# Performance work log

Hardware: AMD Instinct MI355X
Metric: run time of the kernel (lower is better)

## Reference

```python
import jax, jax.numpy as jnp
import numpy as np

B, C, H, W = 16, 512, 64, 64
L, D = 77, 768
NH = 8
HD = C // NH
EPS = 1e-5


def layernorm(x, g, b):
    m = jnp.mean(x, axis=-1, keepdims=True)
    v = jnp.var(x, axis=-1, keepdims=True)
    return (x - m) * jax.lax.rsqrt(v + EPS) * g + b


def setup_inputs() -> dict:
    key = jax.random.key(0)
    ks = jax.random.split(key, 12)
    s_c = 1.0 / np.sqrt(C)
    s_d = 1.0 / np.sqrt(D)
    return {
        "x": jax.random.normal(ks[0], (B, C, H, W), jnp.float32),
        "text_features": jax.random.normal(ks[1], (B, L, D), jnp.float32),
        "wq": jax.random.normal(ks[2], (C, C), jnp.float32) * s_c,
        "bq": jnp.zeros((C,), jnp.float32),
        "wk": jax.random.normal(ks[3], (C, D), jnp.float32) * s_d,
        "bk": jnp.zeros((C,), jnp.float32),
        "wv": jax.random.normal(ks[4], (C, D), jnp.float32) * s_d,
        "bv": jnp.zeros((C,), jnp.float32),
        "wo": jax.random.normal(ks[5], (C, C), jnp.float32) * s_c,
        "bo": jnp.zeros((C,), jnp.float32),
        "g1": jnp.ones((C,), jnp.float32),
        "b1": jnp.zeros((C,), jnp.float32),
        "g2": jnp.ones((C,), jnp.float32),
        "b2": jnp.zeros((C,), jnp.float32),
    }


def reference(x, text_features, wq, bq, wk, bk, wv, bv, wo, bo, g1, b1, g2, b2):
    b, c, h, w = x.shape
    # 1x1 conv query projection
    q = jnp.einsum('bchw,oc->bohw', x, wq) + bq[None, :, None, None]
    # 2D positional encoding: first c/2 channels vary along w, next c/2 along h
    pos_x = jnp.broadcast_to(jnp.linspace(0.0, 1.0, w)[None, :], (h, w))
    pos_y = jnp.broadcast_to(jnp.linspace(0.0, 1.0, h)[:, None], (h, w))
    pe = jnp.concatenate([
        jnp.broadcast_to(pos_x[None], (c // 2, h, w)),
        jnp.broadcast_to(pos_y[None], (c // 2, h, w)),
    ], axis=0)  # [C,H,W]
    q = q + 0.05 * pe[None]
    # flatten spatial -> tokens, layernorm over channels
    q_flat = q.reshape(b, c, h * w).transpose(0, 2, 1)  # [B,HW,C]
    q_norm = layernorm(q_flat, g1, b1)
    qh = q_norm.reshape(b, h * w, NH, HD)  # [B,HW,NH,HD]
    # text key/value projections
    k = jnp.einsum('bld,cd->blc', text_features, wk) + bk
    v = jnp.einsum('bld,cd->blc', text_features, wv) + bv
    k_norm = layernorm(k, g2, b2)
    kh = k_norm.reshape(b, -1, NH, HD)
    vh = v.reshape(b, -1, NH, HD)
    scale = HD ** -0.5
    attn = jnp.einsum('bqhd,bkhd->bhqk', qh, kh) * scale  # [B,NH,HW,L]
    attn = jax.nn.softmax(attn, axis=-1)  # dropout is identity in eval
    out = jnp.einsum('bhqk,bkhd->bqhd', attn, vh).reshape(b, h * w, c)
    out = out.transpose(0, 2, 1).reshape(b, c, h, w)
    out = jnp.einsum('bchw,oc->bohw', out, wo) + bo[None, :, None, None]
    return out + x
```

## Files before the change

kernel.cpp:

```cpp
#include <hip/hip_runtime.h>
#include <stdint.h>

#define BD   16
#define CD   512
#define HD_  64
#define NH_  8
#define HWD  4096
#define LD   77
#define DD   768

typedef __bf16 bf16;
typedef bf16 bf16x8 __attribute__((ext_vector_type(8)));
typedef float f32x4 __attribute__((ext_vector_type(4)));

__device__ __forceinline__ void async16(const bf16* g, bf16* l) {
  __builtin_amdgcn_global_load_lds(
      (const __attribute__((address_space(1))) void*)g,
      (__attribute__((address_space(3))) void*)l, 16, 0, 0);
}

__device__ __forceinline__ unsigned short bfb(float f) {
  bf16 h = (bf16)f;
  return __builtin_bit_cast(unsigned short, h);
}

__global__ __launch_bounds__(256) void xpose_cvt(const float* __restrict__ X,
                                                 bf16* __restrict__ Y) {
  __shared__ float tile[64][68];
  const int b = blockIdx.z, c0 = blockIdx.y * 64, t0 = blockIdx.x * 64;
  const int tid = threadIdx.x;
  const float* Xb = X + ((size_t)b * CD + c0) * HWD + t0;
#pragma unroll
  for (int p = 0; p < 4; ++p) {
    int c = (tid >> 4) + p * 16;
    int t = (tid & 15) * 4;
    float4 v = *(const float4*)(Xb + (size_t)c * HWD + t);
    *(float4*)&tile[c][t] = v;
  }
  __syncthreads();
  int t = tid >> 2, cb = (tid & 3) * 16;
  union { uint4 u[2]; unsigned short us[16]; } pk;
#pragma unroll
  for (int j = 0; j < 16; ++j) pk.us[j] = bfb(tile[cb + j][t]);
  uint4* Yp = (uint4*)(Y + ((size_t)(b * HWD + t0 + t)) * CD + c0 + cb);
  Yp[0] = pk.u[0];
  Yp[1] = pk.u[1];
}

__global__ __launch_bounds__(256) void cvt_all(
    const float* __restrict__ t, const float* __restrict__ q,
    const float* __restrict__ k, const float* __restrict__ v,
    const float* __restrict__ o, bf16* __restrict__ tb, bf16* __restrict__ qb,
    bf16* __restrict__ kb, bf16* __restrict__ vb, bf16* __restrict__ ob) {
  int bid = blockIdx.x;
  const float* src;
  bf16* dst;
  if (bid < 462) { src = t; dst = tb; }
  else if (bid < 590) { src = q; dst = qb; bid -= 462; }
  else if (bid < 782) { src = k; dst = kb; bid -= 590; }
  else if (bid < 974) { src = v; dst = vb; bid -= 782; }
  else { src = o; dst = ob; bid -= 974; }
  int i = (bid * 256 + threadIdx.x) * 8;
  float4 a = *(const float4*)(src + i);
  float4 c = *(const float4*)(src + i + 4);
  union { uint4 u; unsigned short us[8]; } pk;
  pk.us[0] = bfb(a.x); pk.us[1] = bfb(a.y); pk.us[2] = bfb(a.z); pk.us[3] = bfb(a.w);
  pk.us[4] = bfb(c.x); pk.us[5] = bfb(c.y); pk.us[6] = bfb(c.z); pk.us[7] = bfb(c.w);
  *(uint4*)(dst + i) = pk.u;
}

template <int TM, int TN, int MODE>
__global__ __launch_bounds__(256)
void gemm_bt(const bf16* __restrict__ A, const bf16* __restrict__ B,
             int M, int N, int K,
             const float* __restrict__ bias, const float* __restrict__ xres,
             float* __restrict__ D,
             const bf16* __restrict__ B2, const float* __restrict__ bias2,
             float* __restrict__ D2) {
  constexpr int WM = TM / 2, WN = TN / 2;
  constexpr int AFR = WM / 16, BFR = WN / 16;
  constexpr int ACH = TM / 8, TCH = (TM + TN) / 8, WCH = TCH / 4;
  __shared__ bf16 sA[TM * 64];
  __shared__ bf16 sB[TN * 64];
  const int tid = threadIdx.x, wave = tid >> 6, lane = tid & 63;
  const int m0 = blockIdx.y * TM;
  int n0 = blockIdx.x * TN;
  if constexpr (MODE == 2) {
    if (n0 >= (N >> 1)) { B = B2; bias = bias2; D = D2; n0 -= (N >> 1); }
  }
  const int wm = (wave >> 1) * WM, wn = (wave & 1) * WN;
  const int sub = lane >> 3, col8 = (lane & 7) * 8;
  const int mlo = lane & 15, khi = lane >> 4;
  f32x4 acc[AFR][BFR] = {};

  for (int k0 = 0; k0 < K; k0 += 64) {
#pragma unroll
    for (int r = 0; r < WCH; ++r) {
      int ci = wave * WCH + r;
      if (ci < ACH) {
        int row = ci * 8 + sub;
        int g = m0 + row;
        if (g > M - 1) g = M - 1;
        async16(A + (size_t)g * K + k0 + col8, &sA[ci * 512]);
      } else {
        int cj = ci - ACH;
        int row = cj * 8 + sub;
        async16(B + (size_t)(n0 + row) * K + k0 + col8, &sB[cj * 512]);
      }
    }
    __syncthreads();
#pragma unroll
    for (int kc = 0; kc < 2; ++kc) {
      bf16x8 af[AFR], bfv[BFR];
      const int ko = kc * 32 + khi * 8;
#pragma unroll
      for (int i = 0; i < AFR; ++i)
        af[i] = *(const bf16x8*)&sA[(wm + i * 16 + mlo) * 64 + ko];
#pragma unroll
      for (int j = 0; j < BFR; ++j)
        bfv[j] = *(const bf16x8*)&sB[(wn + j * 16 + mlo) * 64 + ko];
#pragma unroll
      for (int i = 0; i < AFR; ++i)
#pragma unroll
        for (int j = 0; j < BFR; ++j)
          acc[i][j] = __builtin_amdgcn_mfma_f32_16x16x32_bf16(af[i], bfv[j],
                                                              acc[i][j], 0, 0, 0);
    }
    __syncthreads();
  }

  if constexpr (MODE == 3) {
    float bn[BFR];
#pragma unroll
    for (int j = 0; j < BFR; ++j) bn[j] = bias[n0 + wn + j * 16 + mlo];
#pragma unroll
    for (int i = 0; i < AFR; ++i) {
      const int m = m0 + wm + i * 16 + khi * 4;
      const int b = m >> 12, hw = m & (HWD - 1);
      const float* xr0 = xres + ((size_t)b * CD) * HWD + hw;
      float* d0 = D + ((size_t)b * CD) * HWD + hw;
#pragma unroll
      for (int j = 0; j < BFR; ++j) {
        const size_t off = (size_t)(n0 + wn + j * 16 + mlo) * HWD;
        float4 xr = *(const float4*)(xr0 + off);
        float4 ov;
        ov.x = acc[i][j][0] + bn[j] + xr.x;
        ov.y = acc[i][j][1] + bn[j] + xr.y;
        ov.z = acc[i][j][2] + bn[j] + xr.z;
        ov.w = acc[i][j][3] + bn[j] + xr.w;
        *(float4*)(d0 + off) = ov;
      }
    }
  } else {
#pragma unroll
    for (int i = 0; i < AFR; ++i) {
      const int mb = m0 + wm + i * 16 + khi * 4;
#pragma unroll
      for (int j = 0; j < BFR; ++j) {
        const int n = n0 + wn + j * 16 + mlo;
#pragma unroll
        for (int r = 0; r < 4; ++r) {
          const int m = mb + r;
          if (m < M) D[(size_t)m * CD + n] = acc[i][j][r] + bias[n];
        }
      }
    }
  }
}

__global__ __launch_bounds__(256) void qgemm_ln(const bf16* __restrict__ A,
                                                const bf16* __restrict__ Bw,
                                                const float* __restrict__ bias,
                                                const float* __restrict__ g1,
                                                const float* __restrict__ b1,
                                                bf16* __restrict__ Y) {
  constexpr int TM = 64, KK = 512;
  constexpr int AFR = 4, BFR = 8;
  __shared__ bf16 sA[TM * 64];
  __shared__ bf16 sB[512 * 64];
  __shared__ float sStat[4][TM][2];
  const int tid = threadIdx.x, wave = tid >> 6, lane = tid & 63;
  const int m0 = blockIdx.x * TM;
  const int wn = wave * 128;
  const int sub = lane >> 3, col8 = (lane & 7) * 8;
  const int mlo = lane & 15, khi = lane >> 4;
  f32x4 acc[AFR][BFR] = {};

  for (int k0 = 0; k0 < KK; k0 += 64) {
#pragma unroll
    for (int r = 0; r < 18; ++r) {
      int ci = wave * 18 + r;
      if (ci < 8) {
        int row = ci * 8 + sub;
        async16(A + (size_t)(m0 + row) * KK + k0 + col8, &sA[ci * 512]);
      } else {
        int cj = ci - 8;
        int row = cj * 8 + sub;
        async16(Bw + (size_t)row * KK + k0 + col8, &sB[cj * 512]);
      }
    }
    __syncthreads();
#pragma unroll
    for (int kc = 0; kc < 2; ++kc) {
      const int ko = kc * 32 + khi * 8;
      bf16x8 af[AFR], bfv[BFR];
#pragma unroll
      for (int i = 0; i < AFR; ++i)
        af[i] = *(const bf16x8*)&sA[(i * 16 + mlo) * 64 + ko];
#pragma unroll
      for (int j = 0; j < BFR; ++j)
        bfv[j] = *(const bf16x8*)&sB[(wn + j * 16 + mlo) * 64 + ko];
#pragma unroll
      for (int i = 0; i < AFR; ++i)
#pragma unroll
        for (int j = 0; j < BFR; ++j)
          acc[i][j] = __builtin_amdgcn_mfma_f32_16x16x32_bf16(af[i], bfv[j],
                                                              acc[i][j], 0, 0, 0);
    }
    __syncthreads();
  }

  float cb[8], cg[8], ct[8];
#pragma unroll
  for (int j = 0; j < 8; ++j) {
    int n = wn + j * 16 + mlo;
    cb[j] = bias[n];
    cg[j] = g1[n];
    ct[j] = b1[n];
  }

#pragma unroll
  for (int i = 0; i < AFR; ++i) {
#pragma unroll
    for (int r = 0; r < 4; ++r) {
      const int row = i * 16 + khi * 4 + r;
      const int hw = (m0 + row) & (HWD - 1);
      const float pex = (float)(hw & 63) * (0.05f / 63.0f);
      const float pey = (float)(hw >> 6) * (0.05f / 63.0f);
      float s = 0.f, sq = 0.f;
#pragma unroll
      for (int j = 0; j < 8; ++j) {
        float v = acc[i][j][r] + cb[j] + ((wn + j * 16) < 256 ? pex : pey);
        acc[i][j][r] = v;
        s += v;
        sq += v * v;
      }
      s += __shfl_xor(s, 1);  sq += __shfl_xor(sq, 1);
      s += __shfl_xor(s, 2);  sq += __shfl_xor(sq, 2);
      s += __shfl_xor(s, 4);  sq += __shfl_xor(sq, 4);
      s += __shfl_xor(s, 8);  sq += __shfl_xor(sq, 8);
      if (mlo == 0) {
        sStat[wave][row][0] = s;
        sStat[wave][row][1] = sq;
      }
    }
  }
  __syncthreads();

#pragma unroll
  for (int i = 0; i < AFR; ++i) {
#pragma unroll
    for (int r = 0; r < 4; ++r) {
      const int row = i * 16 + khi * 4 + r;
      float s = sStat[0][row][0] + sStat[1][row][0] +
                sStat[2][row][0] + sStat[3][row][0];
      float sq = sStat[0][row][1] + sStat[1][row][1] +
                 sStat[2][row][1] + sStat[3][row][1];
      float mean = s * (1.0f / 512.0f);
      float var = sq * (1.0f / 512.0f) - mean * mean;
      float rstd = rsqrtf(var + 1e-5f);
      bf16* yr = Y + (size_t)(m0 + row) * CD + wn + mlo;
#pragma unroll
      for (int j = 0; j < 8; ++j)
        yr[j * 16] = (bf16)((acc[i][j][r] - mean) * rstd * cg[j] + ct[j]);
    }
  }
}

__global__ __launch_bounds__(256) void ln_rows(const float* __restrict__ X,
                                               const float* __restrict__ gg,
                                               const float* __restrict__ bb,
                                               bf16* __restrict__ Y, int nrows,
                                               int khlayout) {
  const int wv = threadIdx.x >> 6, lane = threadIdx.x & 63;
  const int row = blockIdx.x * 4 + wv;
  if (row >= nrows) return;
  const float* xr = X + (size_t)row * CD + lane * 8;
  float4 v0 = *(const float4*)xr;
  float4 v1 = *(const float4*)(xr + 4);
  float xv[8] = {v0.x, v0.y, v0.z, v0.w, v1.x, v1.y, v1.z, v1.w};
  float s = 0.f, sq = 0.f;
#pragma unroll
  for (int j = 0; j < 8; ++j) { s += xv[j]; sq += xv[j] * xv[j]; }
#pragma unroll
  for (int off = 1; off < 64; off <<= 1) {
    s += __shfl_xor(s, off);
    sq += __shfl_xor(sq, off);
  }
  float mean = s * (1.0f / 512.0f);
  float var = sq * (1.0f / 512.0f) - mean * mean;
  float rstd = rsqrtf(var + 1e-5f);
  const int c0 = lane * 8;
  union { uint4 u; unsigned short us[8]; } pk;
#pragma unroll
  for (int j = 0; j < 8; ++j)
    pk.us[j] = bfb((xv[j] - mean) * rstd * gg[c0 + j] + bb[c0 + j]);
  size_t ya;
  if (khlayout) {
    int bq = row / LD, l = row - bq * LD;
    int hh = lane >> 3, dd = (lane & 7) * 8;
    ya = (((size_t)(bq * NH_ + hh)) * LD + l) * HD_ + dd;
  } else {
    ya = (size_t)row * CD + c0;
  }
  *(uint4*)(Y + ya) = pk.u;
}

__global__ __launch_bounds__(256) void make_vt(const float* __restrict__ vraw,
                                               bf16* __restrict__ vt) {
  const int bh = blockIdx.x, b = bh >> 3, h = bh & 7;
  const int tid = threadIdx.x, d = tid & 63, lg = tid >> 6;
  for (int l = lg; l < 96; l += 4) {
    float v = 0.f;
    if (l < LD) v = vraw[((size_t)(b * LD + l)) * CD + h * HD_ + d];
    vt[((size_t)(bh * HD_ + d)) * 96 + l] = (bf16)v;
  }
}

__global__ __launch_bounds__(256) void attn_k(const bf16* __restrict__ Q,
                                              const bf16* __restrict__ KH,
                                              const bf16* __restrict__ VT,
                                              bf16* __restrict__ O) {
  __shared__ bf16 P[4][16 * 104];
  const int tid = threadIdx.x, wv = tid >> 6, lane = tid & 63;
  const int m = lane & 15, kg = lane >> 4;
  const int q0 = blockIdx.x * 64, h = blockIdx.y, b = blockIdx.z;
  const int bh = b * NH_ + h;

  const size_t qoff = ((size_t)(b * HWD + q0 + wv * 16 + m)) * CD + h * HD_;
  bf16x8 a0 = *(const bf16x8*)(Q + qoff + kg * 8);
  bf16x8 a1 = *(const bf16x8*)(Q + qoff + 32 + kg * 8);

  const bf16* Kb = KH + (size_t)bh * LD * HD_;
  f32x4 s[5];
#pragma unroll
  for (int kt = 0; kt < 5; ++kt) {
    int key = kt * 16 + m;
    if (key > LD - 1) key = LD - 1;
    const bf16* kr = Kb + key * HD_ + kg * 8;
    bf16x8 b0 = *(const bf16x8*)kr;
    bf16x8 b1 = *(const bf16x8*)(kr + 32);
    f32x4 z = {0.f, 0.f, 0.f, 0.f};
    z = __builtin_amdgcn_mfma_f32_16x16x32_bf16(a0, b0, z, 0, 0, 0);
    z = __builtin_amdgcn_mfma_f32_16x16x32_bf16(a1, b1, z, 0, 0, 0);
    s[kt] = z;
  }

  bf16* Pw = &P[wv][0];
#pragma unroll
  for (int r = 0; r < 4; ++r) {
    float sc[5];
#pragma unroll
    for (int kt = 0; kt < 5; ++kt) {
      float v = s[kt][r] * 0.125f;
      if (kt == 4 && m >= LD - 64) v = -3.0e38f;
      sc[kt] = v;
    }
    float mx = fmaxf(fmaxf(fmaxf(sc[0], sc[1]), fmaxf(sc[2], sc[3])), sc[4]);
    mx = fmaxf(mx, __shfl_xor(mx, 1));
    mx = fmaxf(mx, __shfl_xor(mx, 2));
    mx = fmaxf(mx, __shfl_xor(mx, 4));
    mx = fmaxf(mx, __shfl_xor(mx, 8));
    float sum = 0.f;
#pragma unroll
    for (int kt = 0; kt < 5; ++kt) {
      sc[kt] = __expf(sc[kt] - mx);
      sum += sc[kt];
    }
    sum += __shfl_xor(sum, 1);
    sum += __shfl_xor(sum, 2);
    sum += __shfl_xor(sum, 4);
    sum += __shfl_xor(sum, 8);
    float inv = 1.0f / sum;
    const int prow = kg * 4 + r;
#pragma unroll
    for (int kt = 0; kt < 5; ++kt)
      Pw[prow * 104 + kt * 16 + m] = (bf16)(sc[kt] * inv);
    Pw[prow * 104 + 80 + m] = (bf16)0.f;
  }
  __syncthreads();

  bf16x8 ap[3];
#pragma unroll
  for (int kc = 0; kc < 3; ++kc)
    ap[kc] = *(const bf16x8*)&Pw[m * 104 + kc * 32 + kg * 8];

  const bf16* Vb = VT + (size_t)bh * HD_ * 96;
  f32x4 o[4] = {};
#pragma unroll
  for (int nt = 0; nt < 4; ++nt) {
#pragma unroll
    for (int kc = 0; kc < 3; ++kc) {
      bf16x8 bv = *(const bf16x8*)(Vb + (nt * 16 + m) * 96 + kc * 32 + kg * 8);
      o[nt] = __builtin_amdgcn_mfma_f32_16x16x32_bf16(ap[kc], bv, o[nt], 0, 0, 0);
    }
  }
#pragma unroll
  for (int nt = 0; nt < 4; ++nt)
#pragma unroll
    for (int r = 0; r < 4; ++r) {
      const int row = b * HWD + q0 + wv * 16 + kg * 4 + r;
      O[(size_t)row * CD + h * HD_ + nt * 16 + m] = (bf16)(o[nt][r]);
    }
}

extern "C" void kernel_launch(void* const* d_in, const int* in_sizes, int n_in,
                              void* d_out, int out_size, void* d_ws, size_t ws_size,
                              hipStream_t stream) {
  const float* x    = (const float*)d_in[0];
  const float* text = (const float*)d_in[1];
  const float* wq   = (const float*)d_in[2];
  const float* bq   = (const float*)d_in[3];
  const float* wk   = (const float*)d_in[4];
  const float* bk   = (const float*)d_in[5];
  const float* wv   = (const float*)d_in[6];
  const float* bv   = (const float*)d_in[7];
  const float* wo   = (const float*)d_in[8];
  const float* bo   = (const float*)d_in[9];
  const float* g1   = (const float*)d_in[10];
  const float* b1   = (const float*)d_in[11];
  const float* g2   = (const float*)d_in[12];
  const float* b2   = (const float*)d_in[13];
  float* out = (float*)d_out;

  char* p = (char*)d_ws;
  auto alloc = [&](size_t bytes) {
    char* r = p;
    p += (bytes + 255) & ~(size_t)255;
    return r;
  };
  bf16* xt     = (bf16*)alloc((size_t)BD * HWD * CD * 2);
  bf16* attn_o = (bf16*)alloc((size_t)BD * HWD * CD * 2);
  bf16* textb  = (bf16*)alloc((size_t)BD * LD * DD * 2);
  bf16* wqb    = (bf16*)alloc((size_t)CD * CD * 2);
  bf16* wkb    = (bf16*)alloc((size_t)CD * DD * 2);
  bf16* wvb    = (bf16*)alloc((size_t)CD * DD * 2);
  bf16* wob    = (bf16*)alloc((size_t)CD * CD * 2);
  float* kraw  = (float*)alloc((size_t)BD * LD * CD * 4);
  float* vraw  = (float*)alloc((size_t)BD * LD * CD * 4);
  bf16* kh     = (bf16*)alloc((size_t)BD * NH_ * LD * HD_ * 2);
  bf16* vt     = (bf16*)alloc((size_t)BD * NH_ * HD_ * 96 * 2);
  bf16* qbf = (bf16*)out;

  xpose_cvt<<<dim3(HWD / 64, CD / 64, BD), 256, 0, stream>>>(x, xt);
  cvt_all<<<1102, 256, 0, stream>>>(text, wq, wk, wv, wo,
                                    textb, wqb, wkb, wvb, wob);

  gemm_bt<128, 128, 2><<<dim3(8, 10), 256, 0, stream>>>(
      textb, wkb, BD * LD, 2 * CD, DD, bk, nullptr, kraw, wvb, bv, vraw);
  ln_rows<<<(BD * LD + 3) / 4, 256, 0, stream>>>(kraw, g2, b2, kh, BD * LD, 1);
  make_vt<<<BD * NH_, 256, 0, stream>>>(vraw, vt);

  qgemm_ln<<<dim3(BD * HWD / 64), 256, 0, stream>>>(xt, wqb, bq, g1, b1, qbf);

  attn_k<<<dim3(HWD / 64, NH_, BD), 256, 0, stream>>>(qbf, kh, vt, attn_o);

  gemm_bt<256, 128, 3><<<dim3(CD / 128, BD * HWD / 256), 256, 0, stream>>>(
      attn_o, wob, BD * HWD, CD, CD, bo, x, out, nullptr, nullptr, nullptr);
}
```

Measured before the change: 581.4 us.

## Split Q-proj LayerNorm into partial stats and apply it inside attention

Replaces the monolithic qgemm_ln kernel, which held all 512 output columns per 64-row block, with the generic 128x128 GEMM. Its epilogue writes un-normalized bf16 Q plus per-128-column partial sum and sum-of-squares. The attention kernel combines the four partials and applies LayerNorm with g1/b1 to its Q fragments before the QK MFMA. The change also flattens the GEMM grid with an XCD-aware block remap and shrinks the output-projection tile to 128x128. This aims to raise occupancy and parallelism in the Q GEMM, at the cost of extra stat traffic and normalizing from bf16-rounded values.

```diff
diff --git a/kernel.cpp b/kernel.cpp
--- a/kernel.cpp
+++ b/kernel.cpp
@@ -69,7 +69,7 @@
   *(uint4*)(dst + i) = pk.u;
 }
 
-template <int TM, int TN, int MODE>
+template <int TM, int TN, int MODE, int NBX>
 __global__ __launch_bounds__(256)
 void gemm_bt(const bf16* __restrict__ A, const bf16* __restrict__ B,
              int M, int N, int K,
@@ -83,8 +83,13 @@
   __shared__ bf16 sA[TM * 64];
   __shared__ bf16 sB[TN * 64];
   const int tid = threadIdx.x, wave = tid >> 6, lane = tid & 63;
-  const int m0 = blockIdx.y * TM;
-  int n0 = blockIdx.x * TN;
+  int flat = blockIdx.x;
+  {
+    const int qq = (int)gridDim.x >> 3;
+    flat = (flat & 7) * qq + (flat >> 3);
+  }
+  const int m0 = (flat / NBX) * TM;
+  int n0 = (flat % NBX) * TN;
   if constexpr (MODE == 2) {
     if (n0 >= (N >> 1)) { B = B2; bias = bias2; D = D2; n0 -= (N >> 1); }
   }
@@ -129,7 +134,45 @@
     __syncthreads();
   }
 
-  if constexpr (MODE == 3) {
+  if constexpr (MODE == 0) {
+    __shared__ float sRS[TM][2][2];
+    bf16* Dq = (bf16*)D;
+    const int wnh = wave & 1;
+#pragma unroll
+    for (int i = 0; i < AFR; ++i) {
+#pragma unroll
+      for (int r = 0; r < 4; ++r) {
+        const int rowt = wm + i * 16 + khi * 4 + r;
+        const int m = m0 + rowt;
+        const int hw = m & (HWD - 1);
+        const float pex = (float)(hw & 63) * (0.05f / 63.0f);
+        const float pey = (float)(hw >> 6) * (0.05f / 63.0f);
+        float s = 0.f, sq = 0.f;
+#pragma unroll
+        for (int j = 0; j < BFR; ++j) {
+          const int n = n0 + wn + j * 16 + mlo;
+          float v = acc[i][j][r] + bias[n] + (n < 256 ? pex : pey);
+          bf16 hv = (bf16)v;
+          Dq[(size_t)m * CD + n] = hv;
+          float vr = (float)hv;
+          s += vr;
+          sq += vr * vr;
+        }
+        s += __shfl_xor(s, 1); sq += __shfl_xor(sq, 1);
+        s += __shfl_xor(s, 2); sq += __shfl_xor(sq, 2);
+        s += __shfl_xor(s, 4); sq += __shfl_xor(sq, 4);
+        s += __shfl_xor(s, 8); sq += __shfl_xor(sq, 8);
+        if (mlo == 0) { sRS[rowt][wnh][0] = s; sRS[rowt][wnh][1] = sq; }
+      }
+    }
+    __syncthreads();
+    if (tid < TM) {
+      float s = sRS[tid][0][0] + sRS[tid][1][0];
+      float sq = sRS[tid][0][1] + sRS[tid][1][1];
+      float2* pst = (float2*)xres;
+      pst[(size_t)(n0 >> 7) * (BD * HWD) + (m0 + tid)] = make_float2(s, sq);
+    }
+  } else if constexpr (MODE == 3) {
     float bn[BFR];
 #pragma unroll
     for (int j = 0; j < BFR; ++j) bn[j] = bias[n0 + wn + j * 16 + mlo];
@@ -164,115 +207,6 @@
           if (m < M) D[(size_t)m * CD + n] = acc[i][j][r] + bias[n];
         }
       }
-    }
-  }
-}
-
-__global__ __launch_bounds__(256) void qgemm_ln(const bf16* __restrict__ A,
-                                                const bf16* __restrict__ Bw,
-                                                const float* __restrict__ bias,
-                                                const float* __restrict__ g1,
-                                                const float* __restrict__ b1,
-                                                bf16* __restrict__ Y) {
-  constexpr int TM = 64, KK = 512;
-  constexpr int AFR = 4, BFR = 8;
-  __shared__ bf16 sA[TM * 64];
-  __shared__ bf16 sB[512 * 64];
-  __shared__ float sStat[4][TM][2];
-  const int tid = threadIdx.x, wave = tid >> 6, lane = tid & 63;
-  const int m0 = blockIdx.x * TM;
-  const int wn = wave * 128;
-  const int sub = lane >> 3, col8 = (lane & 7) * 8;
-  const int mlo = lane & 15, khi = lane >> 4;
-  f32x4 acc[AFR][BFR] = {};
-
-  for (int k0 = 0; k0 < KK; k0 += 64) {
-#pragma unroll
-    for (int r = 0; r < 18; ++r) {
-      int ci = wave * 18 + r;
-      if (ci < 8) {
-        int row = ci * 8 + sub;
-        async16(A + (size_t)(m0 + row) * KK + k0 + col8, &sA[ci * 512]);
-      } else {
-        int cj = ci - 8;
-        int row = cj * 8 + sub;
-        async16(Bw + (size_t)row * KK + k0 + col8, &sB[cj * 512]);
-      }
-    }
-    __syncthreads();
-#pragma unroll
-    for (int kc = 0; kc < 2; ++kc) {
-      const int ko = kc * 32 + khi * 8;
-      bf16x8 af[AFR], bfv[BFR];
-#pragma unroll
-      for (int i = 0; i < AFR; ++i)
-        af[i] = *(const bf16x8*)&sA[(i * 16 + mlo) * 64 + ko];
-#pragma unroll
-      for (int j = 0; j < BFR; ++j)
-        bfv[j] = *(const bf16x8*)&sB[(wn + j * 16 + mlo) * 64 + ko];
-#pragma unroll
-      for (int i = 0; i < AFR; ++i)
-#pragma unroll
-        for (int j = 0; j < BFR; ++j)
-          acc[i][j] = __builtin_amdgcn_mfma_f32_16x16x32_bf16(af[i], bfv[j],
-                                                              acc[i][j], 0, 0, 0);
-    }
-    __syncthreads();
-  }
-
-  float cb[8], cg[8], ct[8];
-#pragma unroll
-  for (int j = 0; j < 8; ++j) {
-    int n = wn + j * 16 + mlo;
-    cb[j] = bias[n];
-    cg[j] = g1[n];
-    ct[j] = b1[n];
-  }
-
-#pragma unroll
-  for (int i = 0; i < AFR; ++i) {
-#pragma unroll
-    for (int r = 0; r < 4; ++r) {
-      const int row = i * 16 + khi * 4 + r;
-      const int hw = (m0 + row) & (HWD - 1);
-      const float pex = (float)(hw & 63) * (0.05f / 63.0f);
-      const float pey = (float)(hw >> 6) * (0.05f / 63.0f);
-      float s = 0.f, sq = 0.f;
-#pragma unroll
-      for (int j = 0; j < 8; ++j) {
-        float v = acc[i][j][r] + cb[j] + ((wn + j * 16) < 256 ? pex : pey);
-        acc[i][j][r] = v;
-        s += v;
-        sq += v * v;
-      }
-      s += __shfl_xor(s, 1);  sq += __shfl_xor(sq, 1);
-      s += __shfl_xor(s, 2);  sq += __shfl_xor(sq, 2);
-      s += __shfl_xor(s, 4);  sq += __shfl_xor(sq, 4);
-      s += __shfl_xor(s, 8);  sq += __shfl_xor(sq, 8);
-      if (mlo == 0) {
-        sStat[wave][row][0] = s;
-        sStat[wave][row][1] = sq;
-      }
-    }
-  }
-  __syncthreads();
-
-#pragma unroll
-  for (int i = 0; i < AFR; ++i) {
-#pragma unroll
-    for (int r = 0; r < 4; ++r) {
-      const int row = i * 16 + khi * 4 + r;
-      float s = sStat[0][row][0] + sStat[1][row][0] +
-                sStat[2][row][0] + sStat[3][row][0];
-      float sq = sStat[0][row][1] + sStat[1][row][1] +
-                 sStat[2][row][1] + sStat[3][row][1];
-      float mean = s * (1.0f / 512.0f);
-      float var = sq * (1.0f / 512.0f) - mean * mean;
-      float rstd = rsqrtf(var + 1e-5f);
-      bf16* yr = Y + (size_t)(m0 + row) * CD + wn + mlo;
-#pragma unroll
-      for (int j = 0; j < 8; ++j)
-        yr[j * 16] = (bf16)((acc[i][j][r] - mean) * rstd * cg[j] + ct[j]);
     }
   }
 }
@@ -328,6 +262,9 @@
 }
 
 __global__ __launch_bounds__(256) void attn_k(const bf16* __restrict__ Q,
+                                              const float2* __restrict__ PST,
+                                              const float* __restrict__ G1,
+                                              const float* __restrict__ B1,
                                               const bf16* __restrict__ KH,
                                               const bf16* __restrict__ VT,
                                               bf16* __restrict__ O) {
@@ -337,12 +274,37 @@
   const int q0 = blockIdx.x * 64, h = blockIdx.y, b = blockIdx.z;
   const int bh = b * NH_ + h;
 
-  const size_t qoff = ((size_t)(b * HWD + q0 + wv * 16 + m)) * CD + h * HD_;
-  bf16x8 a0 = *(const bf16x8*)(Q + qoff + kg * 8);
-  bf16x8 a1 = *(const bf16x8*)(Q + qoff + 32 + kg * 8);
+  const int rowg = b * HWD + q0 + wv * 16 + m;
+  const size_t qoff = (size_t)rowg * CD + h * HD_;
+  bf16x8 a0r = *(const bf16x8*)(Q + qoff + kg * 8);
+  bf16x8 a1r = *(const bf16x8*)(Q + qoff + 32 + kg * 8);
+
+  float2 st = PST[(size_t)kg * (BD * HWD) + rowg];
+  float s = st.x, sq = st.y;
+  s += __shfl_xor(s, 16); sq += __shfl_xor(sq, 16);
+  s += __shfl_xor(s, 32); sq += __shfl_xor(sq, 32);
+  const float mean = s * (1.0f / 512.0f);
+  const float var = sq * (1.0f / 512.0f) - mean * mean;
+  const float rstd = rsqrtf(var + 1e-5f);
+
+  const int c0 = h * HD_ + kg * 8;
+  float4 ga = *(const float4*)(G1 + c0), gb = *(const float4*)(G1 + c0 + 4);
+  float4 gc = *(const float4*)(G1 + c0 + 32), gd = *(const float4*)(G1 + c0 + 36);
+  float4 ta = *(const float4*)(B1 + c0), tb = *(const float4*)(B1 + c0 + 4);
+  float4 tc = *(const float4*)(B1 + c0 + 32), td = *(const float4*)(B1 + c0 + 36);
+  const float gg[16] = {ga.x, ga.y, ga.z, ga.w, gb.x, gb.y, gb.z, gb.w,
+                        gc.x, gc.y, gc.z, gc.w, gd.x, gd.y, gd.z, gd.w};
+  const float bbv[16] = {ta.x, ta.y, ta.z, ta.w, tb.x, tb.y, tb.z, tb.w,
+                         tc.x, tc.y, tc.z, tc.w, td.x, td.y, td.z, td.w};
+  bf16x8 a0, a1;
+#pragma unroll
+  for (int e = 0; e < 8; ++e) {
+    a0[e] = (bf16)(((float)a0r[e] - mean) * rstd * gg[e] + bbv[e]);
+    a1[e] = (bf16)(((float)a1r[e] - mean) * rstd * gg[8 + e] + bbv[8 + e]);
+  }
 
   const bf16* Kb = KH + (size_t)bh * LD * HD_;
-  f32x4 s[5];
+  f32x4 sacc[5];
 #pragma unroll
   for (int kt = 0; kt < 5; ++kt) {
     int key = kt * 16 + m;
@@ -353,7 +315,7 @@
     f32x4 z = {0.f, 0.f, 0.f, 0.f};
     z = __builtin_amdgcn_mfma_f32_16x16x32_bf16(a0, b0, z, 0, 0, 0);
     z = __builtin_amdgcn_mfma_f32_16x16x32_bf16(a1, b1, z, 0, 0, 0);
-    s[kt] = z;
+    sacc[kt] = z;
   }
 
   bf16* Pw = &P[wv][0];
@@ -362,7 +324,7 @@
     float sc[5];
 #pragma unroll
     for (int kt = 0; kt < 5; ++kt) {
-      float v = s[kt][r] * 0.125f;
+      float v = sacc[kt][r] * 0.125f;
       if (kt == 4 && m >= LD - 64) v = -3.0e38f;
       sc[kt] = v;
     }
@@ -450,21 +412,25 @@
   float* vraw  = (float*)alloc((size_t)BD * LD * CD * 4);
   bf16* kh     = (bf16*)alloc((size_t)BD * NH_ * LD * HD_ * 2);
   bf16* vt     = (bf16*)alloc((size_t)BD * NH_ * HD_ * 96 * 2);
+  float* pstat = (float*)alloc((size_t)4 * BD * HWD * 2 * 4);
   bf16* qbf = (bf16*)out;
 
   xpose_cvt<<<dim3(HWD / 64, CD / 64, BD), 256, 0, stream>>>(x, xt);
   cvt_all<<<1102, 256, 0, stream>>>(text, wq, wk, wv, wo,
                                     textb, wqb, wkb, wvb, wob);
 
-  gemm_bt<128, 128, 2><<<dim3(8, 10), 256, 0, stream>>>(
+  gemm_bt<128, 128, 2, 8><<<80, 256, 0, stream>>>(
       textb, wkb, BD * LD, 2 * CD, DD, bk, nullptr, kraw, wvb, bv, vraw);
   ln_rows<<<(BD * LD + 3) / 4, 256, 0, stream>>>(kraw, g2, b2, kh, BD * LD, 1);
   make_vt<<<BD * NH_, 256, 0, stream>>>(vraw, vt);
 
-  qgemm_ln<<<dim3(BD * HWD / 64), 256, 0, stream>>>(xt, wqb, bq, g1, b1, qbf);
-
-  attn_k<<<dim3(HWD / 64, NH_, BD), 256, 0, stream>>>(qbf, kh, vt, attn_o);
-
-  gemm_bt<256, 128, 3><<<dim3(CD / 128, BD * HWD / 256), 256, 0, stream>>>(
+  gemm_bt<128, 128, 0, 4><<<2048, 256, 0, stream>>>(
+      xt, wqb, BD * HWD, CD, CD, bq, pstat, (float*)qbf,
+      nullptr, nullptr, nullptr);
+
+  attn_k<<<dim3(HWD / 64, NH_, BD), 256, 0, stream>>>(
+      qbf, (const float2*)pstat, g1, b1, kh, vt, attn_o);
+
+  gemm_bt<128, 128, 3, 4><<<2048, 256, 0, stream>>>(
       attn_o, wob, BD * HWD, CD, CD, bo, x, out, nullptr, nullptr, nullptr);
 }
```

After: 557.6 us. -4.1%, faster.
